# Optimization experiments

Hardware: AMD Instinct MI355X
Metric: run time of the kernel (lower is better)

## Reference

```python
import jax, jax.numpy as jnp
import numpy as np

N = 20000      # nodes
E = 320000     # edges (avg degree 16)
F_IN = 256     # input feature dim
HID = 128      # hidden_channels
H1 = 4         # heads layer 1
ED = 26        # edge feature dim
OUT = 128      # out_channels


def _layernorm(x, g, b, eps=1e-5):
    mu = jnp.mean(x, axis=-1, keepdims=True)
    var = jnp.var(x, axis=-1, keepdims=True)
    return (x - mu) * jax.lax.rsqrt(var + eps) * g + b


def _gatv2(x, src, dst, ea, Wl, bl, Wr, br, We, att, bias, n, heads, c, concat):
    # PyG GATv2Conv: lin_l on source nodes, lin_r on target nodes, lin_edge (no bias)
    xl = (x @ Wl + bl).reshape(n, heads, c)          # [N,H,C] source transform
    xr = (x @ Wr + br).reshape(n, heads, c)          # [N,H,C] target transform
    m = xl[src] + xr[dst] + (ea @ We).reshape(-1, heads, c)  # [E,H,C]
    m = jax.nn.leaky_relu(m, 0.2)
    alpha = jnp.einsum('ehc,hc->eh', m, att)          # [E,H]
    amax = jax.ops.segment_max(alpha, dst, num_segments=n)
    ex = jnp.exp(alpha - amax[dst])
    den = jax.ops.segment_sum(ex, dst, num_segments=n)[dst] + 1e-16
    a = ex / den                                      # scatter-softmax over in-edges
    out = jax.ops.segment_sum(xl[src] * a[:, :, None], dst, num_segments=n)  # [N,H,C]
    out = out.reshape(n, heads * c) if concat else out.mean(axis=1)
    return out + bias


def setup_inputs() -> dict:
    key = jax.random.key(0)
    ks = jax.random.split(key, 30)
    r = lambda k, s, sc=0.05: jax.random.normal(k, s, jnp.float32) * sc
    D1 = HID * H1  # 512
    return {
        'x': r(ks[0], (N, F_IN), 1.0),
        'edge_index': jax.random.randint(ks[1], (2, E), 0, N),
        'edge_attr': r(ks[2], (E, ED), 1.0),
        # conv1 (heads=4, concat)
        'W1l': r(ks[3], (F_IN, D1)), 'b1l': jnp.zeros((D1,), jnp.float32),
        'W1r': r(ks[4], (F_IN, D1)), 'b1r': jnp.zeros((D1,), jnp.float32),
        'We1': r(ks[5], (ED, D1)),
        'att1': r(ks[6], (H1, HID)),
        'bias1': jnp.zeros((D1,), jnp.float32),
        'Wskip1': r(ks[7], (F_IN, D1)), 'bskip1': jnp.zeros((D1,), jnp.float32),
        'g1': jnp.ones((D1,), jnp.float32), 'be1': jnp.zeros((D1,), jnp.float32),
        # conv2 (heads=1, mean)
        'W2l': r(ks[8], (D1, OUT)), 'b2l': jnp.zeros((OUT,), jnp.float32),
        'W2r': r(ks[9], (D1, OUT)), 'b2r': jnp.zeros((OUT,), jnp.float32),
        'We2': r(ks[10], (ED, OUT)),
        'att2': r(ks[11], (1, OUT)),
        'bias2': jnp.zeros((OUT,), jnp.float32),
        'Wskip2': r(ks[12], (D1, OUT)), 'bskip2': jnp.zeros((OUT,), jnp.float32),
        'g2': jnp.ones((OUT,), jnp.float32), 'be2': jnp.zeros((OUT,), jnp.float32),
    }


def reference(x, edge_index, edge_attr, W1l, b1l, W1r, b1r, We1, att1, bias1,
              Wskip1, bskip1, g1, be1, W2l, b2l, W2r, b2r, We2, att2, bias2,
              Wskip2, bskip2, g2, be2):
    src, dst = edge_index[0], edge_index[1]
    h = _gatv2(x, src, dst, edge_attr, W1l, b1l, W1r, b1r, We1, att1, bias1,
               N, H1, HID, True)
    h = h + (x @ Wskip1 + bskip1)
    h = jax.nn.elu(_layernorm(h, g1, be1))  # dropout is identity in eval
    h2 = _gatv2(h, src, dst, edge_attr, W2l, b2l, W2r, b2r, We2, att2, bias2,
                N, 1, OUT, False)
    h2 = h2 + (h @ Wskip2 + bskip2)
    return _layernorm(h2, g2, be2)
```

## Files before the change

kernel.cpp:

```cpp
#include <hip/hip_runtime.h>
#include <hip/hip_bf16.h>

typedef __bf16 bf16;
typedef __bf16 v8bf __attribute__((ext_vector_type(8)));
typedef float f32x4 __attribute__((ext_vector_type(4)));
typedef float f32x2 __attribute__((ext_vector_type(2)));

#define NN 20000
#define EE 320000
#define FIN 256
#define D1 512
#define DOUT 128
#define ED 26

__device__ __forceinline__ float b2f(bf16 x) { return (float)x; }

__device__ __forceinline__ f32x2 ldbf2v(const bf16* p) {
  unsigned int u;
  __builtin_memcpy(&u, p, 4);
  union { unsigned int i; float f; } lo, hi;
  lo.i = (u & 0xffffu) << 16;
  hi.i = u & 0xffff0000u;
  return (f32x2){lo.f, hi.f};
}

__device__ __forceinline__ f32x2 ldf2v(const float* p) {
  f32x2 t;
  __builtin_memcpy(&t, p, 8);
  return t;
}

__device__ __forceinline__ f32x4 ldf4v(const float* p) {
  f32x4 t;
  __builtin_memcpy(&t, p, 16);
  return t;
}

__global__ void zero_k(int* __restrict__ p, int n) {
  int i = blockIdx.x * 256 + threadIdx.x;
  if (i < n) p[i] = 0;
}

__global__ void detflag_k(const int* __restrict__ ei32, int* __restrict__ flag) {
  int i = blockIdx.x * 256 + threadIdx.x;
  int v = (i < EE) ? ei32[2 * i + 1] : 0;
  unsigned long long b = __ballot(v != 0);
  if ((threadIdx.x & 63) == 0 && b) atomicOr(flag, 1);
}

__global__ void conv_k(const void* __restrict__ ei, const int* __restrict__ flag,
                       int* __restrict__ src, int* __restrict__ dst) {
  int i = blockIdx.x * 256 + threadIdx.x;
  if (i >= EE) return;
  int s, d;
  if (*flag == 0) {
    const long long* p = (const long long*)ei;
    s = (int)p[i];
    d = (int)p[EE + i];
  } else {
    const int* p = (const int*)ei;
    s = p[i];
    d = p[EE + i];
  }
  src[i] = min(max(s, 0), NN - 1);
  dst[i] = min(max(d, 0), NN - 1);
}

__global__ void hist_k(const int* __restrict__ dst, int* __restrict__ deg, int n) {
  int e = blockIdx.x * 256 + threadIdx.x;
  if (e < n) atomicAdd(&deg[dst[e]], 1);
}

__global__ __launch_bounds__(1024) void scan_k(const int* __restrict__ deg,
                                               int* __restrict__ offs,
                                               int* __restrict__ cursor, int n) {
  __shared__ int lsum[1024];
  int t = threadIdx.x;
  const int CH = (n + 1023) / 1024;
  int base = t * CH;
  int s = 0;
  for (int i = 0; i < CH; i++) {
    int idx = base + i;
    if (idx < n) s += deg[idx];
  }
  lsum[t] = s;
  __syncthreads();
  for (int o = 1; o < 1024; o <<= 1) {
    int v = (t >= o) ? lsum[t - o] : 0;
    __syncthreads();
    lsum[t] += v;
    __syncthreads();
  }
  int ex = (t == 0) ? 0 : lsum[t - 1];
  for (int i = 0; i < CH; i++) {
    int idx = base + i;
    if (idx < n) {
      offs[idx] = ex;
      cursor[idx] = ex;
      ex += deg[idx];
    }
  }
  if (t == 1023) offs[n] = lsum[1023];
}

__global__ void scatter_k(const int* __restrict__ dst, int* __restrict__ cursor,
                          int* __restrict__ elist, int n) {
  int e = blockIdx.x * 256 + threadIdx.x;
  if (e < n) {
    int p = atomicAdd(&cursor[dst[e]], 1);
    if ((unsigned)p < (unsigned)EE) elist[p] = e;
  }
}

__global__ __launch_bounds__(256) void egather_k(
    const float* __restrict__ eatt, const int* __restrict__ elist,
    const int* __restrict__ srcs, const int* __restrict__ dsts,
    bf16* __restrict__ ea_csr, int* __restrict__ s_csr,
    int* __restrict__ d_csr) {
  __shared__ int e_s[128];
  int tid = threadIdx.x;
  int base = blockIdx.x * 128;
  if (tid < 128) {
    int e = elist[base + tid];
    e = min(max(e, 0), EE - 1);
    e_s[tid] = e;
    s_csr[base + tid] = srcs[e];
    d_csr[base + tid] = dsts[e];
  }
  __syncthreads();
  for (int idx = tid; idx < 128 * 32; idx += 256) {
    int i = idx >> 5, k = idx & 31;
    float v = (k < 26) ? eatt[(size_t)e_s[i] * ED + k] : 0.f;
    ea_csr[(size_t)(base + i) * 32 + k] = (bf16)v;
  }
}

__global__ __launch_bounds__(256) void xpack_k(const float* __restrict__ x,
                                               bf16* __restrict__ xbf,
                                               long long n8) {
  long long i = (long long)blockIdx.x * 256 + threadIdx.x;
  if (i >= n8) return;
  const float* ap = x + i * 8;
  f32x4 u, v;
  __builtin_memcpy(&u, ap, 16);
  __builtin_memcpy(&v, ap + 4, 16);
  v8bf o;
#pragma unroll
  for (int j = 0; j < 4; j++) {
    o[j] = (bf16)u[j];
    o[4 + j] = (bf16)v[j];
  }
  __builtin_memcpy(xbf + i * 8, &o, 16);
}

__global__ __launch_bounds__(256) void packT_k(const float* __restrict__ W,
                                               bf16* __restrict__ Bp,
                                               int Nc, int K) {
  __shared__ float t[32][33];
  int c0 = blockIdx.x * 32, k0 = blockIdx.y * 32;
  int tr = threadIdx.x >> 5, tc = threadIdx.x & 31;
#pragma unroll
  for (int i = 0; i < 32; i += 8)
    t[tr + i][tc] = W[(size_t)(k0 + tr + i) * Nc + c0 + tc];
  __syncthreads();
#pragma unroll
  for (int i = 0; i < 32; i += 8)
    Bp[(size_t)(c0 + tr + i) * K + k0 + tc] = (bf16)t[tc][tr + i];
}

__global__ __launch_bounds__(256) void packWe_k(const float* __restrict__ We,
                                                bf16* __restrict__ Wp, int Nc) {
  int o = blockIdx.x * 256 + threadIdx.x;
  int j = o & 7;
  int lc = (o >> 3) & 15;
  int quad = (o >> 7) & 3;
  int ng = o >> 9;
  int k = quad * 8 + j;
  int col = ng * 16 + lc;
  float v = (k < 26) ? We[(size_t)k * Nc + col] : 0.f;
  Wp[o] = (bf16)v;
}

template <typename TA, typename TO, bool ADD>
__global__ __launch_bounds__(256) void gemm_t(const TA* __restrict__ A,
                                              const float* __restrict__ B,
                                              const float* __restrict__ bias,
                                              TO* out, int Nc, int K) {
  int w = threadIdx.x >> 6;
  int l = threadIdx.x & 63;
  int quad = l >> 4;
  int mrow = blockIdx.y * 16 + (l & 15);
  int col = blockIdx.x * 64 + w * 16 + (l & 15);
  f32x4 acc = {0.f, 0.f, 0.f, 0.f};
  for (int k0 = 0; k0 < K; k0 += 32) {
    int ka = k0 + quad * 8;
    v8bf a, b;
    if constexpr (sizeof(TA) == 4) {
      const float* ap = (const float*)A + (size_t)mrow * K + ka;
#pragma unroll
      for (int j = 0; j < 8; j++) a[j] = (bf16)ap[j];
    } else {
      __builtin_memcpy(&a, (const bf16*)A + (size_t)mrow * K + ka, 16);
    }
#pragma unroll
    for (int j = 0; j < 8; j++) b[j] = (bf16)B[(size_t)(ka + j) * Nc + col];
    acc = __builtin_amdgcn_mfma_f32_16x16x32_bf16(a, b, acc, 0, 0, 0);
  }
  float bb = bias[col];
  int obase = blockIdx.y * 16 + quad * 4;
#pragma unroll
  for (int r = 0; r < 4; r++) {
    size_t idx = (size_t)(obase + r) * Nc + col;
    float v = acc[r] + bb;
    if (ADD) v += (float)out[idx];
    out[idx] = (TO)v;
  }
}

template <typename TA, typename TO>
__global__ __launch_bounds__(256) void gemm2_t(const TA* __restrict__ A,
                                               const float* __restrict__ B0,
                                               const float* __restrict__ B1,
                                               const float* __restrict__ bias0,
                                               const float* __restrict__ bias1,
                                               TO* __restrict__ out0,
                                               TO* __restrict__ out1,
                                               int Nc, int K) {
  int w = threadIdx.x >> 6;
  int l = threadIdx.x & 63;
  int quad = l >> 4;
  int mrow = blockIdx.y * 16 + (l & 15);
  int col = blockIdx.x * 64 + w * 16 + (l & 15);
  f32x4 acc0 = {0.f, 0.f, 0.f, 0.f};
  f32x4 acc1 = {0.f, 0.f, 0.f, 0.f};
  for (int k0 = 0; k0 < K; k0 += 32) {
    int ka = k0 + quad * 8;
    v8bf a, b0, b1;
    if constexpr (sizeof(TA) == 4) {
      const float* ap = (const float*)A + (size_t)mrow * K + ka;
#pragma unroll
      for (int j = 0; j < 8; j++) a[j] = (bf16)ap[j];
    } else {
      __builtin_memcpy(&a, (const bf16*)A + (size_t)mrow * K + ka, 16);
    }
#pragma unroll
    for (int j = 0; j < 8; j++) {
      size_t bi = (size_t)(ka + j) * Nc + col;
      b0[j] = (bf16)B0[bi];
      b1[j] = (bf16)B1[bi];
    }
    acc0 = __builtin_amdgcn_mfma_f32_16x16x32_bf16(a, b0, acc0, 0, 0, 0);
    acc1 = __builtin_amdgcn_mfma_f32_16x16x32_bf16(a, b1, acc1, 0, 0, 0);
  }
  float bb0 = bias0[col], bb1 = bias1[col];
  int obase = blockIdx.y * 16 + quad * 4;
#pragma unroll
  for (int r = 0; r < 4; r++) {
    size_t idx = (size_t)(obase + r) * Nc + col;
    out0[idx] = (TO)(acc0[r] + bb0);
    out1[idx] = (TO)(acc1[r] + bb1);
  }
}

template <typename TA, typename TO>
__global__ __launch_bounds__(256) void gemm3p_t(
    const TA* __restrict__ A, const bf16* __restrict__ Bp,
    const float* __restrict__ bias0, const float* __restrict__ bias1,
    const float* __restrict__ bias2, TO* __restrict__ out0,
    TO* __restrict__ out1, TO* __restrict__ out2, int Nc, int K, int M) {
  int w = threadIdx.x >> 6;
  int l = threadIdx.x & 63;
  int quad = l >> 4, lc = l & 15;
  int col = blockIdx.x * 64 + w * 16 + lc;
  int mbase = blockIdx.y * 64;
  const bf16* b0p = Bp + (size_t)col * K;
  const bf16* b1p = Bp + ((size_t)Nc + col) * K;
  const bf16* b2p = Bp + ((size_t)2 * Nc + col) * K;
  f32x4 acc[4][3];
#pragma unroll
  for (int i = 0; i < 4; i++)
#pragma unroll
    for (int j = 0; j < 3; j++) acc[i][j] = (f32x4){0.f, 0.f, 0.f, 0.f};
  for (int k0 = 0; k0 < K; k0 += 32) {
    int ka = k0 + quad * 8;
    v8bf b0, b1, b2;
    __builtin_memcpy(&b0, b0p + ka, 16);
    __builtin_memcpy(&b1, b1p + ka, 16);
    __builtin_memcpy(&b2, b2p + ka, 16);
#pragma unroll
    for (int ms = 0; ms < 4; ms++) {
      int row = min(mbase + ms * 16 + lc, M - 1);
      v8bf a;
      if constexpr (sizeof(TA) == 4) {
        const float* ap = (const float*)A + (size_t)row * K + ka;
        f32x4 u, v;
        __builtin_memcpy(&u, ap, 16);
        __builtin_memcpy(&v, ap + 4, 16);
#pragma unroll
        for (int j = 0; j < 4; j++) {
          a[j] = (bf16)u[j];
          a[4 + j] = (bf16)v[j];
        }
      } else {
        __builtin_memcpy(&a, (const bf16*)A + (size_t)row * K + ka, 16);
      }
      acc[ms][0] = __builtin_amdgcn_mfma_f32_16x16x32_bf16(a, b0, acc[ms][0], 0, 0, 0);
      acc[ms][1] = __builtin_amdgcn_mfma_f32_16x16x32_bf16(a, b1, acc[ms][1], 0, 0, 0);
      acc[ms][2] = __builtin_amdgcn_mfma_f32_16x16x32_bf16(a, b2, acc[ms][2], 0, 0, 0);
    }
  }
  float bb0 = bias0[col], bb1 = bias1[col], bb2 = bias2[col];
#pragma unroll
  for (int ms = 0; ms < 4; ms++) {
    int ob = mbase + ms * 16 + quad * 4;
#pragma unroll
    for (int r = 0; r < 4; r++) {
      int orow = ob + r;
      if (orow < M) {
        size_t idx = (size_t)orow * Nc + col;
        out0[idx] = (TO)(acc[ms][0][r] + bb0);
        out1[idx] = (TO)(acc[ms][1][r] + bb1);
        out2[idx] = (TO)(acc[ms][2][r] + bb2);
      }
    }
  }
}

__global__ __launch_bounds__(256) void alpha1c_k(
    const bf16* __restrict__ xl, const bf16* __restrict__ xr,
    const bf16* __restrict__ ea_csr, const bf16* __restrict__ Wp,
    const float* __restrict__ att, const int* __restrict__ s_csr,
    const int* __restrict__ d_csr, float* __restrict__ alphap) {
  __shared__ bf16 ea_s[128 * 40];
  int tid = threadIdx.x;
  int w = __builtin_amdgcn_readfirstlane(tid >> 6);
  int l = tid & 63;
  int quad = l >> 4, lc = l & 15;
  int base = blockIdx.x * 128;
  for (int idx = tid; idx < 1024; idx += 256) {
    int i = idx >> 3, k4 = (idx & 7) * 4;
    unsigned long long v;
    __builtin_memcpy(&v, ea_csr + (size_t)(base + i) * 32 + k4, 8);
    __builtin_memcpy(&ea_s[i * 40 + k4], &v, 8);
  }
  int c0 = w * 128;
  v8bf bfrag[8];
  float av[8];
#pragma unroll
  for (int n = 0; n < 8; n++) {
    int col = c0 + n * 16 + lc;
    av[n] = att[col];
    __builtin_memcpy(&bfrag[n],
                     Wp + ((size_t)((w * 8 + n) * 4 + quad) * 16 + lc) * 8, 16);
  }
  __syncthreads();
#pragma unroll 1
  for (int m = 0; m < 8; m++) {
    v8bf afrag;
    __builtin_memcpy(&afrag, &ea_s[(m * 16 + lc) * 40 + quad * 8], 16);
    f32x4 z = {0.f, 0.f, 0.f, 0.f};
    f32x4 acc[8];
#pragma unroll
    for (int n = 0; n < 8; n++)
      acc[n] = __builtin_amdgcn_mfma_f32_16x16x32_bf16(afrag, bfrag[n], z, 0, 0, 0);
    int e0 = base + m * 16 + quad * 4;
    int sA[4], dA[4];
#pragma unroll
    for (int r = 0; r < 4; r++) {
      sA[r] = s_csr[e0 + r];
      dA[r] = d_csr[e0 + r];
    }
    f32x4 pal = {0.f, 0.f, 0.f, 0.f};
#pragma unroll
    for (int n = 0; n < 8; n++) {
      int col = c0 + n * 16 + lc;
#pragma unroll
      for (int r = 0; r < 4; r++) {
        float mm = (float)xl[(size_t)sA[r] * D1 + col] +
                   (float)xr[(size_t)dA[r] * D1 + col] + acc[n][r];
        mm = fmaxf(mm, 0.f) + 0.2f * fminf(mm, 0.f);
        pal[r] += mm * av[n];
      }
    }
#pragma unroll
    for (int o = 1; o < 16; o <<= 1) {
      pal[0] += __shfl_xor(pal[0], o, 64);
      pal[1] += __shfl_xor(pal[1], o, 64);
      pal[2] += __shfl_xor(pal[2], o, 64);
      pal[3] += __shfl_xor(pal[3], o, 64);
    }
    if (lc == 0) {
#pragma unroll
      for (int r = 0; r < 4; r++) alphap[(size_t)(e0 + r) * 4 + w] = pal[r];
    }
  }
}

__global__ __launch_bounds__(256) void alpha2c_k(
    const float* __restrict__ xl, const float* __restrict__ xr,
    const bf16* __restrict__ ea_csr, const bf16* __restrict__ Wp,
    const float* __restrict__ att, const int* __restrict__ s_csr,
    const int* __restrict__ d_csr, float* __restrict__ alphap) {
  __shared__ bf16 ea_s[128 * 40];
  __shared__ float pal_s[4 * 128];
  int tid = threadIdx.x;
  int w = __builtin_amdgcn_readfirstlane(tid >> 6);
  int l = tid & 63;
  int quad = l >> 4, lc = l & 15;
  int base = blockIdx.x * 128;
  for (int idx = tid; idx < 1024; idx += 256) {
    int i = idx >> 3, k4 = (idx & 7) * 4;
    unsigned long long v;
    __builtin_memcpy(&v, ea_csr + (size_t)(base + i) * 32 + k4, 8);
    __builtin_memcpy(&ea_s[i * 40 + k4], &v, 8);
  }
  int c0 = w * 32;
  v8bf bfrag[2];
  float av[2];
#pragma unroll
  for (int n = 0; n < 2; n++) {
    int col = c0 + n * 16 + lc;
    av[n] = att[col];
    __builtin_memcpy(&bfrag[n],
                     Wp + ((size_t)((w * 2 + n) * 4 + quad) * 16 + lc) * 8, 16);
  }
  __syncthreads();
#pragma unroll 1
  for (int m = 0; m < 8; m++) {
    v8bf afrag;
    __builtin_memcpy(&afrag, &ea_s[(m * 16 + lc) * 40 + quad * 8], 16);
    f32x4 z = {0.f, 0.f, 0.f, 0.f};
    f32x4 acc[2];
#pragma unroll
    for (int n = 0; n < 2; n++)
      acc[n] = __builtin_amdgcn_mfma_f32_16x16x32_bf16(afrag, bfrag[n], z, 0, 0, 0);
    int e0 = base + m * 16 + quad * 4;
    int sA[4], dA[4];
#pragma unroll
    for (int r = 0; r < 4; r++) {
      sA[r] = s_csr[e0 + r];
      dA[r] = d_csr[e0 + r];
    }
    f32x4 pal = {0.f, 0.f, 0.f, 0.f};
#pragma unroll
    for (int n = 0; n < 2; n++) {
      int col = c0 + n * 16 + lc;
#pragma unroll
      for (int r = 0; r < 4; r++) {
        float mm = xl[(size_t)sA[r] * DOUT + col] +
                   xr[(size_t)dA[r] * DOUT + col] + acc[n][r];
        mm = fmaxf(mm, 0.f) + 0.2f * fminf(mm, 0.f);
        pal[r] += mm * av[n];
      }
    }
#pragma unroll
    for (int o = 1; o < 16; o <<= 1) {
      pal[0] += __shfl_xor(pal[0], o, 64);
      pal[1] += __shfl_xor(pal[1], o, 64);
      pal[2] += __shfl_xor(pal[2], o, 64);
      pal[3] += __shfl_xor(pal[3], o, 64);
    }
    if (lc == 0) {
      int eb = m * 16 + quad * 4;
#pragma unroll
      for (int r = 0; r < 4; r++) pal_s[w * 128 + eb + r] = pal[r];
    }
  }
  __syncthreads();
  if (tid < 128) {
    float a = pal_s[tid] + pal_s[128 + tid] + pal_s[256 + tid] + pal_s[384 + tid];
    alphap[base + tid] = a;
  }
}

__global__ __launch_bounds__(256) void agg1c_k(
    const bf16* __restrict__ xl, const bf16* __restrict__ skip,
    const float* __restrict__ alphap, const float* __restrict__ bias,
    const float* __restrict__ g, const float* __restrict__ be,
    const int* __restrict__ s_csr, const int* __restrict__ offs,
    bf16* __restrict__ hout) {
  int tid = threadIdx.x;
  int w = tid >> 6, l = tid & 63;
  int node = blockIdx.x * 4 + w;
  if (node >= NN) return;
  int c = l * 8;
  int head = l >> 4;
  int i0 = offs[node], i1 = offs[node + 1];
  i0 = max(0, min(i0, EE));
  i1 = max(i0, min(i1, EE));
  float m = -3.0e38f;
  for (int i = i0 + (l & 15); i < i1; i += 16)
    m = fmaxf(m, alphap[(size_t)i * 4 + head]);
#pragma unroll
  for (int o = 1; o < 16; o <<= 1) m = fmaxf(m, __shfl_xor(m, o, 64));
  float den = 0.f;
  f32x4 a0 = {0.f, 0.f, 0.f, 0.f}, a1 = {0.f, 0.f, 0.f, 0.f};
  int s = 0;
  float al = 0.f;
  if (i0 < i1) {
    s = __builtin_amdgcn_readfirstlane(s_csr[i0]);
    al = alphap[(size_t)i0 * 4 + head];
  }
  for (int i = i0; i < i1; i++) {
    int s_n = s;
    float al_n = al;
    if (i + 1 < i1) {
      s_n = __builtin_amdgcn_readfirstlane(s_csr[i + 1]);
      al_n = alphap[(size_t)(i + 1) * 4 + head];
    }
    float pr = __expf(al - m);
    den += pr;
    v8bf xv;
    __builtin_memcpy(&xv, xl + (size_t)s * D1 + c, 16);
#pragma unroll
    for (int j = 0; j < 4; j++) {
      a0[j] += pr * (float)xv[j];
      a1[j] += pr * (float)xv[4 + j];
    }
    s = s_n;
    al = al_n;
  }
  float inv = 1.f / (den + 1e-16f);
  v8bf skv;
  __builtin_memcpy(&skv, skip + (size_t)node * D1 + c, 16);
  f32x4 bv0 = ldf4v(bias + c), bv1 = ldf4v(bias + c + 4);
  float o[8];
#pragma unroll
  for (int j = 0; j < 4; j++) {
    o[j] = a0[j] * inv + bv0[j] + (float)skv[j];
    o[4 + j] = a1[j] * inv + bv1[j] + (float)skv[4 + j];
  }
  float s1 = 0.f, s2 = 0.f;
#pragma unroll
  for (int j = 0; j < 8; j++) {
    s1 += o[j];
    s2 += o[j] * o[j];
  }
#pragma unroll
  for (int of = 32; of; of >>= 1) {
    s1 += __shfl_xor(s1, of, 64);
    s2 += __shfl_xor(s2, of, 64);
  }
  float mu = s1 * (1.f / 512.f);
  float var = fmaxf(s2 * (1.f / 512.f) - mu * mu, 0.f);
  float rs = rsqrtf(var + 1e-5f);
  f32x4 gv0 = ldf4v(g + c), gv1 = ldf4v(g + c + 4);
  f32x4 ev0 = ldf4v(be + c), ev1 = ldf4v(be + c + 4);
  v8bf hv;
#pragma unroll
  for (int j = 0; j < 4; j++) {
    float y0 = (o[j] - mu) * rs * gv0[j] + ev0[j];
    float y1 = (o[4 + j] - mu) * rs * gv1[j] + ev1[j];
    y0 = y0 > 0.f ? y0 : __expf(fminf(y0, 0.f)) - 1.f;
    y1 = y1 > 0.f ? y1 : __expf(fminf(y1, 0.f)) - 1.f;
    hv[j] = (bf16)y0;
    hv[4 + j] = (bf16)y1;
  }
  __builtin_memcpy(hout + (size_t)node * D1 + c, &hv, 16);
}

__global__ __launch_bounds__(256) void agg2c_k(
    const float* __restrict__ xl, const float* __restrict__ skip,
    const float* __restrict__ alphap, const float* __restrict__ bias,
    const float* __restrict__ g, const float* __restrict__ be,
    const int* __restrict__ s_csr, const int* __restrict__ offs,
    float* __restrict__ outp) {
  int tid = threadIdx.x;
  int w = tid >> 6, l = tid & 63;
  int node = blockIdx.x * 4 + w;
  if (node >= NN) return;
  int c = 2 * l;
  int i0 = offs[node], i1 = offs[node + 1];
  i0 = max(0, min(i0, EE));
  i1 = max(i0, min(i1, EE));
  float m = -3.0e38f;
  for (int i = i0 + l; i < i1; i += 64) m = fmaxf(m, alphap[i]);
#pragma unroll
  for (int o = 32; o; o >>= 1) m = fmaxf(m, __shfl_xor(m, o, 64));
  float den = 0.f;
  f32x2 acc = {0.f, 0.f};
  int s = 0;
  float al = 0.f;
  if (i0 < i1) {
    s = __builtin_amdgcn_readfirstlane(s_csr[i0]);
    al = alphap[i0];
  }
  for (int i = i0; i < i1; i++) {
    int s_n = s;
    float al_n = al;
    if (i + 1 < i1) {
      s_n = __builtin_amdgcn_readfirstlane(s_csr[i + 1]);
      al_n = alphap[i + 1];
    }
    float pr = __expf(al - m);
    den += pr;
    f32x2 xv = ldf2v(xl + (size_t)s * DOUT + c);
    acc += (f32x2){pr, pr} * xv;
    s = s_n;
    al = al_n;
  }
  float inv = 1.f / (den + 1e-16f);
  f32x2 sk = ldf2v(skip + (size_t)node * DOUT + c);
  float o0 = acc.x * inv + bias[c] + sk.x;
  float o1 = acc.y * inv + bias[c + 1] + sk.y;
  float s1 = o0 + o1, s2 = o0 * o0 + o1 * o1;
#pragma unroll
  for (int of = 32; of; of >>= 1) {
    s1 += __shfl_xor(s1, of, 64);
    s2 += __shfl_xor(s2, of, 64);
  }
  float mu = s1 * (1.f / 128.f);
  float var = fmaxf(s2 * (1.f / 128.f) - mu * mu, 0.f);
  float rs = rsqrtf(var + 1e-5f);
  outp[(size_t)node * DOUT + c] = (o0 - mu) * rs * g[c] + be[c];
  outp[(size_t)node * DOUT + c + 1] = (o1 - mu) * rs * g[c + 1] + be[c + 1];
}

__global__ __launch_bounds__(256) void alpha1_k(
    const bf16* __restrict__ xl, const bf16* __restrict__ xr,
    const float* __restrict__ eatt, const float* __restrict__ We,
    const float* __restrict__ att, const int* __restrict__ srcs,
    const int* __restrict__ dsts, float* __restrict__ alpha) {
  __shared__ bf16 ea_s[128 * 40];
  int tid = threadIdx.x;
  int w = __builtin_amdgcn_readfirstlane(tid >> 6);
  int l = tid & 63;
  int quad = l >> 4, lc = l & 15;
  int base = blockIdx.x * 128;
  for (int i = tid; i < 128 * 32; i += 256) {
    int e = i >> 5, k = i & 31;
    float v = (k < 26) ? eatt[(size_t)(base + e) * ED + k] : 0.f;
    ea_s[e * 40 + k] = (bf16)v;
  }
  int c0 = w * 128;
  v8bf bfrag[8];
  float av[8];
#pragma unroll
  for (int n = 0; n < 8; n++) {
    int col = c0 + n * 16 + lc;
    av[n] = att[col];
#pragma unroll
    for (int j = 0; j < 8; j++) {
      int k = quad * 8 + j;
      bfrag[n][j] = (k < 26) ? (bf16)We[(size_t)k * D1 + col] : (bf16)0.f;
    }
  }
  __syncthreads();
#pragma unroll 1
  for (int m = 0; m < 8; m++) {
    v8bf afrag;
    __builtin_memcpy(&afrag, &ea_s[(m * 16 + lc) * 40 + quad * 8], 16);
    f32x4 z = {0.f, 0.f, 0.f, 0.f};
    f32x4 acc[8];
#pragma unroll
    for (int n = 0; n < 8; n++)
      acc[n] = __builtin_amdgcn_mfma_f32_16x16x32_bf16(afrag, bfrag[n], z, 0, 0, 0);
    int e0 = base + m * 16 + quad * 4;
    int sA[4], dA[4];
#pragma unroll
    for (int r = 0; r < 4; r++) {
      sA[r] = srcs[e0 + r];
      dA[r] = dsts[e0 + r];
    }
    f32x4 pal = {0.f, 0.f, 0.f, 0.f};
#pragma unroll
    for (int n = 0; n < 8; n++) {
      int col = c0 + n * 16 + lc;
#pragma unroll
      for (int r = 0; r < 4; r++) {
        float mm = (float)xl[(size_t)sA[r] * D1 + col] +
                   (float)xr[(size_t)dA[r] * D1 + col] + acc[n][r];
        mm = fmaxf(mm, 0.f) + 0.2f * fminf(mm, 0.f);
        pal[r] += mm * av[n];
      }
    }
#pragma unroll
    for (int o = 1; o < 16; o <<= 1) {
      pal[0] += __shfl_xor(pal[0], o, 64);
      pal[1] += __shfl_xor(pal[1], o, 64);
      pal[2] += __shfl_xor(pal[2], o, 64);
      pal[3] += __shfl_xor(pal[3], o, 64);
    }
    if (lc == 0) {
#pragma unroll
      for (int r = 0; r < 4; r++) alpha[(size_t)(e0 + r) * 4 + w] = pal[r];
    }
  }
}

__global__ __launch_bounds__(256) void alpha2_k(
    const float* __restrict__ xl, const float* __restrict__ xr,
    const float* __restrict__ eatt, const float* __restrict__ We,
    const float* __restrict__ att, const int* __restrict__ srcs,
    const int* __restrict__ dsts, float* __restrict__ alpha) {
  __shared__ bf16 ea_s[128 * 40];
  __shared__ float pal_s[4 * 128];
  int tid = threadIdx.x;
  int w = __builtin_amdgcn_readfirstlane(tid >> 6);
  int l = tid & 63;
  int quad = l >> 4, lc = l & 15;
  int base = blockIdx.x * 128;
  for (int i = tid; i < 128 * 32; i += 256) {
    int e = i >> 5, k = i & 31;
    float v = (k < 26) ? eatt[(size_t)(base + e) * ED + k] : 0.f;
    ea_s[e * 40 + k] = (bf16)v;
  }
  int c0 = w * 32;
  v8bf bfrag[2];
  float av[2];
#pragma unroll
  for (int n = 0; n < 2; n++) {
    int col = c0 + n * 16 + lc;
    av[n] = att[col];
#pragma unroll
    for (int j = 0; j < 8; j++) {
      int k = quad * 8 + j;
      bfrag[n][j] = (k < 26) ? (bf16)We[(size_t)k * DOUT + col] : (bf16)0.f;
    }
  }
  __syncthreads();
#pragma unroll 1
  for (int m = 0; m < 8; m++) {
    v8bf afrag;
    __builtin_memcpy(&afrag, &ea_s[(m * 16 + lc) * 40 + quad * 8], 16);
    f32x4 z = {0.f, 0.f, 0.f, 0.f};
    f32x4 acc[2];
#pragma unroll
    for (int n = 0; n < 2; n++)
      acc[n] = __builtin_amdgcn_mfma_f32_16x16x32_bf16(afrag, bfrag[n], z, 0, 0, 0);
    int e0 = base + m * 16 + quad * 4;
    int sA[4], dA[4];
#pragma unroll
    for (int r = 0; r < 4; r++) {
      sA[r] = srcs[e0 + r];
      dA[r] = dsts[e0 + r];
    }
    f32x4 pal = {0.f, 0.f, 0.f, 0.f};
#pragma unroll
    for (int n = 0; n < 2; n++) {
      int col = c0 + n * 16 + lc;
#pragma unroll
      for (int r = 0; r < 4; r++) {
        float mm = xl[(size_t)sA[r] * DOUT + col] +
                   xr[(size_t)dA[r] * DOUT + col] + acc[n][r];
        mm = fmaxf(mm, 0.f) + 0.2f * fminf(mm, 0.f);
        pal[r] += mm * av[n];
      }
    }
#pragma unroll
    for (int o = 1; o < 16; o <<= 1) {
      pal[0] += __shfl_xor(pal[0], o, 64);
      pal[1] += __shfl_xor(pal[1], o, 64);
      pal[2] += __shfl_xor(pal[2], o, 64);
      pal[3] += __shfl_xor(pal[3], o, 64);
    }
    if (lc == 0) {
      int eb = m * 16 + quad * 4;
#pragma unroll
      for (int r = 0; r < 4; r++) pal_s[w * 128 + eb + r] = pal[r];
    }
  }
  __syncthreads();
  if (tid < 128) {
    float a = pal_s[tid] + pal_s[128 + tid] + pal_s[256 + tid] + pal_s[384 + tid];
    alpha[base + tid] = a;
  }
}

__global__ __launch_bounds__(256) void agg1_k(
    const bf16* __restrict__ xl, const bf16* __restrict__ skip,
    const float* __restrict__ alpha, const float* __restrict__ bias,
    const float* __restrict__ g, const float* __restrict__ be,
    const int* __restrict__ srcs, const int* __restrict__ offs,
    const int* __restrict__ elist, bf16* __restrict__ hout) {
  int tid = threadIdx.x;
  int w = tid >> 6, l = tid & 63;
  int node = blockIdx.x * 4 + w;
  if (node >= NN) return;
  int c = l * 8;
  int head = l >> 4;
  int i0 = offs[node], i1 = offs[node + 1];
  i0 = max(0, min(i0, EE));
  i1 = max(i0, min(i1, EE));
  float m = -3.0e38f;
  for (int i = i0; i < i1; i++) {
    int e = __builtin_amdgcn_readfirstlane(elist[i]);
    m = fmaxf(m, alpha[(size_t)e * 4 + head]);
  }
  float den = 0.f;
  f32x4 a0 = {0.f, 0.f, 0.f, 0.f}, a1 = {0.f, 0.f, 0.f, 0.f};
  int s = 0;
  float al = 0.f;
  if (i0 < i1) {
    int e = __builtin_amdgcn_readfirstlane(elist[i0]);
    s = __builtin_amdgcn_readfirstlane(srcs[e]);
    al = alpha[(size_t)e * 4 + head];
  }
  for (int i = i0; i < i1; i++) {
    int s_n = s;
    float al_n = al;
    if (i + 1 < i1) {
      int e = __builtin_amdgcn_readfirstlane(elist[i + 1]);
      s_n = __builtin_amdgcn_readfirstlane(srcs[e]);
      al_n = alpha[(size_t)e * 4 + head];
    }
    float pr = __expf(al - m);
    den += pr;
    v8bf xv;
    __builtin_memcpy(&xv, xl + (size_t)s * D1 + c, 16);
#pragma unroll
    for (int j = 0; j < 4; j++) {
      a0[j] += pr * (float)xv[j];
      a1[j] += pr * (float)xv[4 + j];
    }
    s = s_n;
    al = al_n;
  }
  float inv = 1.f / (den + 1e-16f);
  v8bf skv;
  __builtin_memcpy(&skv, skip + (size_t)node * D1 + c, 16);
  f32x4 bv0 = ldf4v(bias + c), bv1 = ldf4v(bias + c + 4);
  float o[8];
#pragma unroll
  for (int j = 0; j < 4; j++) {
    o[j] = a0[j] * inv + bv0[j] + (float)skv[j];
    o[4 + j] = a1[j] * inv + bv1[j] + (float)skv[4 + j];
  }
  float s1 = 0.f, s2 = 0.f;
#pragma unroll
  for (int j = 0; j < 8; j++) {
    s1 += o[j];
    s2 += o[j] * o[j];
  }
#pragma unroll
  for (int of = 32; of; of >>= 1) {
    s1 += __shfl_xor(s1, of, 64);
    s2 += __shfl_xor(s2, of, 64);
  }
  float mu = s1 * (1.f / 512.f);
  float var = fmaxf(s2 * (1.f / 512.f) - mu * mu, 0.f);
  float rs = rsqrtf(var + 1e-5f);
  f32x4 gv0 = ldf4v(g + c), gv1 = ldf4v(g + c + 4);
  f32x4 ev0 = ldf4v(be + c), ev1 = ldf4v(be + c + 4);
  v8bf hv;
#pragma unroll
  for (int j = 0; j < 4; j++) {
    float y0 = (o[j] - mu) * rs * gv0[j] + ev0[j];
    float y1 = (o[4 + j] - mu) * rs * gv1[j] + ev1[j];
    y0 = y0 > 0.f ? y0 : __expf(fminf(y0, 0.f)) - 1.f;
    y1 = y1 > 0.f ? y1 : __expf(fminf(y1, 0.f)) - 1.f;
    hv[j] = (bf16)y0;
    hv[4 + j] = (bf16)y1;
  }
  __builtin_memcpy(hout + (size_t)node * D1 + c, &hv, 16);
}

__global__ __launch_bounds__(256) void agg2_k(
    const float* __restrict__ xl, const float* __restrict__ skip,
    const float* __restrict__ alpha, const float* __restrict__ bias,
    const float* __restrict__ g, const float* __restrict__ be,
    const int* __restrict__ srcs, const int* __restrict__ offs,
    const int* __restrict__ elist, float* __restrict__ outp) {
  int tid = threadIdx.x;
  int w = tid >> 6, l = tid & 63;
  int node = blockIdx.x * 4 + w;
  if (node >= NN) return;
  int c = 2 * l;
  int i0 = offs[node], i1 = offs[node + 1];
  i0 = max(0, min(i0, EE));
  i1 = max(i0, min(i1, EE));
  float m = -3.0e38f;
  for (int i = i0; i < i1; i++) {
    int e = __builtin_amdgcn_readfirstlane(elist[i]);
    m = fmaxf(m, alpha[e]);
  }
  float den = 0.f;
  f32x2 acc = {0.f, 0.f};
  int s = 0;
  float al = 0.f;
  if (i0 < i1) {
    int e = __builtin_amdgcn_readfirstlane(elist[i0]);
    s = __builtin_amdgcn_readfirstlane(srcs[e]);
    al = alpha[e];
  }
  for (int i = i0; i < i1; i++) {
    int s_n = s;
    float al_n = al;
    if (i + 1 < i1) {
      int e = __builtin_amdgcn_readfirstlane(elist[i + 1]);
      s_n = __builtin_amdgcn_readfirstlane(srcs[e]);
      al_n = alpha[e];
    }
    float pr = __expf(al - m);
    den += pr;
    f32x2 xv = ldf2v(xl + (size_t)s * DOUT + c);
    acc += (f32x2){pr, pr} * xv;
    s = s_n;
    al = al_n;
  }
  float inv = 1.f / (den + 1e-16f);
  f32x2 sk = ldf2v(skip + (size_t)node * DOUT + c);
  float o0 = acc.x * inv + bias[c] + sk.x;
  float o1 = acc.y * inv + bias[c + 1] + sk.y;
  float s1 = o0 + o1, s2 = o0 * o0 + o1 * o1;
#pragma unroll
  for (int of = 32; of; of >>= 1) {
    s1 += __shfl_xor(s1, of, 64);
    s2 += __shfl_xor(s2, of, 64);
  }
  float mu = s1 * (1.f / 128.f);
  float var = fmaxf(s2 * (1.f / 128.f) - mu * mu, 0.f);
  float rs = rsqrtf(var + 1e-5f);
  outp[(size_t)node * DOUT + c] = (o0 - mu) * rs * g[c] + be[c];
  outp[(size_t)node * DOUT + c + 1] = (o1 - mu) * rs * g[c + 1] + be[c + 1];
}

__global__ __launch_bounds__(256) void l1_agg(
    const bf16* __restrict__ xl, const bf16* xr,
    const float* __restrict__ eatt, const float* __restrict__ We,
    const float* __restrict__ att, const float* __restrict__ bias,
    const int* __restrict__ srcs, const int* __restrict__ offs,
    const int* __restrict__ elist, bf16* hout) {
  int node = blockIdx.x;
  int tid = threadIdx.x;
  int w = tid >> 6, l = tid & 63;
  int c = w * 128 + 2 * l;
  f32x2 we[ED];
#pragma unroll
  for (int j = 0; j < ED; j++) {
    we[j] = (f32x2){We[(size_t)j * D1 + c], We[(size_t)j * D1 + c + 1]};
  }
  f32x2 av = ldf2v(att + c);
  f32x2 rv = ldbf2v(xr + (size_t)node * D1 + c);
  float m = -3.0e38f, den = 0.f;
  f32x2 acc = {0.f, 0.f};
  int i0 = offs[node], i1 = offs[node + 1];
  i0 = max(0, min(i0, EE));
  i1 = max(i0, min(i1, EE));
  int e = 0, s = 0;
  if (i0 < i1) {
    e = __builtin_amdgcn_readfirstlane(elist[i0]);
    s = __builtin_amdgcn_readfirstlane(srcs[e]);
  }
  for (int i = i0; i < i1; i++) {
    int e_n = e, s_n = s;
    if (i + 1 < i1) {
      e_n = __builtin_amdgcn_readfirstlane(elist[i + 1]);
      s_n = __builtin_amdgcn_readfirstlane(srcs[e_n]);
    }
    f32x2 xv = ldbf2v(xl + (size_t)s * D1 + c);
    const float* ear = eatt + (size_t)e * ED;
    f32x2 et = {0.f, 0.f};
#pragma unroll
    for (int j = 0; j < ED; j += 2) {
      f32x2 t = ldf2v(ear + j);
      et += (f32x2){t.x, t.x} * we[j];
      et += (f32x2){t.y, t.y} * we[j + 1];
    }
    f32x2 mm = xv + rv + et;
    f32x2 pos = {fmaxf(mm.x, 0.f), fmaxf(mm.y, 0.f)};
    f32x2 neg = {fminf(mm.x, 0.f), fminf(mm.y, 0.f)};
    mm = pos + 0.2f * neg;
    float al = mm.x * av.x + mm.y * av.y;
#pragma unroll
    for (int o = 32; o; o >>= 1) al += __shfl_xor(al, o, 64);
    float nm = fmaxf(m, al);
    float sc = __expf(m - nm);
    float pr = __expf(al - nm);
    den = den * sc + pr;
    acc = acc * sc + (f32x2){pr, pr} * xv;
    m = nm;
    e = e_n;
    s = s_n;
  }
  float inv = 1.f / (den + 1e-16f);
  hout[(size_t)node * D1 + c] = (bf16)(acc.x * inv + bias[c]);
  hout[(size_t)node * D1 + c + 1] = (bf16)(acc.y * inv + bias[c + 1]);
}

__global__ __launch_bounds__(256) void l2_agg(
    const float* __restrict__ xl, const float* xr,
    const float* __restrict__ eatt, const float* __restrict__ We,
    const float* __restrict__ att, const float* __restrict__ bias,
    const int* __restrict__ srcs, const int* __restrict__ offs,
    const int* __restrict__ elist, float* hout) {
  int tid = threadIdx.x;
  int w = tid >> 6, l = tid & 63;
  int node = blockIdx.x * 4 + w;
  if (node >= NN) return;
  int c = 2 * l;
  f32x2 we[ED];
#pragma unroll
  for (int j = 0; j < ED; j++) {
    we[j] = (f32x2){We[(size_t)j * DOUT + c], We[(size_t)j * DOUT + c + 1]};
  }
  f32x2 av = ldf2v(att + c);
  f32x2 rv = ldf2v(xr + (size_t)node * DOUT + c);
  float m = -3.0e38f, den = 0.f;
  f32x2 acc = {0.f, 0.f};
  int i0 = offs[node], i1 = offs[node + 1];
  i0 = max(0, min(i0, EE));
  i1 = max(i0, min(i1, EE));
  int e = 0, s = 0;
  if (i0 < i1) {
    e = __builtin_amdgcn_readfirstlane(elist[i0]);
    s = __builtin_amdgcn_readfirstlane(srcs[e]);
  }
  for (int i = i0; i < i1; i++) {
    int e_n = e, s_n = s;
    if (i + 1 < i1) {
      e_n = __builtin_amdgcn_readfirstlane(elist[i + 1]);
      s_n = __builtin_amdgcn_readfirstlane(srcs[e_n]);
    }
    f32x2 xv = ldf2v(xl + (size_t)s * DOUT + c);
    const float* ear = eatt + (size_t)e * ED;
    f32x2 et = {0.f, 0.f};
#pragma unroll
    for (int j = 0; j < ED; j += 2) {
      f32x2 t = ldf2v(ear + j);
      et += (f32x2){t.x, t.x} * we[j];
      et += (f32x2){t.y, t.y} * we[j + 1];
    }
    f32x2 mm = xv + rv + et;
    f32x2 pos = {fmaxf(mm.x, 0.f), fmaxf(mm.y, 0.f)};
    f32x2 neg = {fminf(mm.x, 0.f), fminf(mm.y, 0.f)};
    mm = pos + 0.2f * neg;
    float al = mm.x * av.x + mm.y * av.y;
#pragma unroll
    for (int o = 32; o; o >>= 1) al += __shfl_xor(al, o, 64);
    float nm = fmaxf(m, al);
    float sc = __expf(m - nm);
    float pr = __expf(al - nm);
    den = den * sc + pr;
    acc = acc * sc + (f32x2){pr, pr} * xv;
    m = nm;
    e = e_n;
    s = s_n;
  }
  float inv = 1.f / (den + 1e-16f);
  hout[(size_t)node * DOUT + c] = acc.x * inv + bias[c];
  hout[(size_t)node * DOUT + c + 1] = acc.y * inv + bias[c + 1];
}

__global__ __launch_bounds__(256) void lnelu_k(bf16* buf,
                                               const float* __restrict__ g,
                                               const float* __restrict__ be) {
  int node = blockIdx.x, tid = threadIdx.x;
  int w = tid >> 6, l = tid & 63;
  int c = tid * 2;
  f32x2 o = ldbf2v(buf + (size_t)node * D1 + c);
  float s1 = o.x + o.y, s2 = o.x * o.x + o.y * o.y;
#pragma unroll
  for (int of = 32; of; of >>= 1) {
    s1 += __shfl_xor(s1, of, 64);
    s2 += __shfl_xor(s2, of, 64);
  }
  __shared__ float r1[4], r2[4];
  if (l == 0) { r1[w] = s1; r2[w] = s2; }
  __syncthreads();
  float S1 = r1[0] + r1[1] + r1[2] + r1[3];
  float S2 = r2[0] + r2[1] + r2[2] + r2[3];
  float mu = S1 * (1.f / 512.f);
  float var = fmaxf(S2 * (1.f / 512.f) - mu * mu, 0.f);
  float rs = rsqrtf(var + 1e-5f);
  float y0 = (o.x - mu) * rs * g[c] + be[c];
  float y1 = (o.y - mu) * rs * g[c + 1] + be[c + 1];
  y0 = y0 > 0.f ? y0 : __expf(fminf(y0, 0.f)) - 1.f;
  y1 = y1 > 0.f ? y1 : __expf(fminf(y1, 0.f)) - 1.f;
  buf[(size_t)node * D1 + c] = (bf16)y0;
  buf[(size_t)node * D1 + c + 1] = (bf16)y1;
}

__global__ __launch_bounds__(256) void ln128_k(const float* __restrict__ buf,
                                               const float* __restrict__ g,
                                               const float* __restrict__ be,
                                               float* __restrict__ outp) {
  int tid = threadIdx.x;
  int w = tid >> 6, l = tid & 63;
  int node = blockIdx.x * 4 + w;
  if (node >= NN) return;
  int c = 2 * l;
  f32x2 o = ldf2v(buf + (size_t)node * DOUT + c);
  float s1 = o.x + o.y, s2 = o.x * o.x + o.y * o.y;
#pragma unroll
  for (int of = 32; of; of >>= 1) {
    s1 += __shfl_xor(s1, of, 64);
    s2 += __shfl_xor(s2, of, 64);
  }
  float mu = s1 * (1.f / 128.f);
  float var = fmaxf(s2 * (1.f / 128.f) - mu * mu, 0.f);
  float rs = rsqrtf(var + 1e-5f);
  outp[(size_t)node * DOUT + c] = (o.x - mu) * rs * g[c] + be[c];
  outp[(size_t)node * DOUT + c + 1] = (o.y - mu) * rs * g[c + 1] + be[c + 1];
}

extern "C" void kernel_launch(void* const* d_in, const int* in_sizes, int n_in,
                              void* d_out, int out_size, void* d_ws, size_t ws_size,
                              hipStream_t stream) {
  const float* x = (const float*)d_in[0];
  const void* ei = d_in[1];
  const float* eattr = (const float*)d_in[2];
  const float* W1l = (const float*)d_in[3];
  const float* b1l = (const float*)d_in[4];
  const float* W1r = (const float*)d_in[5];
  const float* b1r = (const float*)d_in[6];
  const float* We1 = (const float*)d_in[7];
  const float* att1 = (const float*)d_in[8];
  const float* bias1 = (const float*)d_in[9];
  const float* Wsk1 = (const float*)d_in[10];
  const float* bsk1 = (const float*)d_in[11];
  const float* g1 = (const float*)d_in[12];
  const float* be1 = (const float*)d_in[13];
  const float* W2l = (const float*)d_in[14];
  const float* b2l = (const float*)d_in[15];
  const float* W2r = (const float*)d_in[16];
  const float* b2r = (const float*)d_in[17];
  const float* We2 = (const float*)d_in[18];
  const float* att2 = (const float*)d_in[19];
  const float* bias2 = (const float*)d_in[20];
  const float* Wsk2 = (const float*)d_in[21];
  const float* bsk2 = (const float*)d_in[22];
  const float* g2 = (const float*)d_in[23];
  const float* be2 = (const float*)d_in[24];

  char* p = (char*)d_ws;
  size_t off = 0;
  auto carve = [&](size_t bytes) {
    void* r = p + off;
    off = (off + bytes + 255) & ~(size_t)255;
    return r;
  };
  int* flag = (int*)carve(sizeof(int));
  int* srcD = (int*)carve(EE * sizeof(int));
  int* dstD = (int*)carve(EE * sizeof(int));
  int* deg = (int*)carve(NN * sizeof(int));
  int* offs = (int*)carve((NN + 1) * sizeof(int));
  int* cursor = (int*)carve(NN * sizeof(int));
  int* elist = (int*)carve(EE * sizeof(int));
  bf16* bufA = (bf16*)carve((size_t)NN * D1 * 2);
  bf16* bufB = (bf16*)carve((size_t)NN * D1 * 2);
  size_t base_need = off;
  bf16* bufC = (bf16*)carve((size_t)NN * D1 * 2);
  bool fused = (off <= ws_size);
  bf16* eacsr = (bf16*)carve((size_t)EE * 32 * 2);
  int* s_csr = (int*)carve(EE * sizeof(int));
  int* d_csr = (int*)carve(EE * sizeof(int));
  bool fused2 = (off <= ws_size);
  bf16* xbf = (bf16*)carve((size_t)NN * FIN * 2);
  bool fused3 = (off <= ws_size);

  float* q0 = (float*)bufA;
  float* q1 = q0 + (size_t)NN * DOUT;
  float* sk2 = (float*)bufC;
  float* alph1 = (float*)d_out;
  float* alph2 = (float*)bufB;
  bf16* W1p = (bf16*)((char*)d_out + 5120000);
  bf16* W2p = W1p + (size_t)3 * D1 * FIN;
  bf16* Wep1 = W2p + (size_t)3 * DOUT * D1;
  bf16* Wep2 = Wep1 + 16384;

  zero_k<<<1, 256, 0, stream>>>(flag, 1);
  detflag_k<<<(EE + 255) / 256, 256, 0, stream>>>((const int*)ei, flag);
  conv_k<<<(EE + 255) / 256, 256, 0, stream>>>(ei, flag, srcD, dstD);

  zero_k<<<(NN + 255) / 256, 256, 0, stream>>>(deg, NN);
  hist_k<<<(EE + 255) / 256, 256, 0, stream>>>(dstD, deg, EE);
  scan_k<<<1, 1024, 0, stream>>>(deg, offs, cursor, NN);
  scatter_k<<<(EE + 255) / 256, 256, 0, stream>>>(dstD, cursor, elist, EE);

  if (fused) {
    packT_k<<<dim3(D1 / 32, FIN / 32), 256, 0, stream>>>(W1l, W1p, D1, FIN);
    packT_k<<<dim3(D1 / 32, FIN / 32), 256, 0, stream>>>(
        W1r, W1p + (size_t)D1 * FIN, D1, FIN);
    packT_k<<<dim3(D1 / 32, FIN / 32), 256, 0, stream>>>(
        Wsk1, W1p + (size_t)2 * D1 * FIN, D1, FIN);
    packT_k<<<dim3(DOUT / 32, D1 / 32), 256, 0, stream>>>(W2l, W2p, DOUT, D1);
    packT_k<<<dim3(DOUT / 32, D1 / 32), 256, 0, stream>>>(
        W2r, W2p + (size_t)DOUT * D1, DOUT, D1);
    packT_k<<<dim3(DOUT / 32, D1 / 32), 256, 0, stream>>>(
        Wsk2, W2p + (size_t)2 * DOUT * D1, DOUT, D1);
    packWe_k<<<64, 256, 0, stream>>>(We1, Wep1, D1);
    packWe_k<<<16, 256, 0, stream>>>(We2, Wep2, DOUT);
    if (fused3) {
      const long long n8 = (long long)NN * FIN / 8;
      xpack_k<<<(unsigned)((n8 + 255) / 256), 256, 0, stream>>>(x, xbf, n8);
      gemm3p_t<bf16, bf16><<<dim3(D1 / 64, (NN + 63) / 64), 256, 0, stream>>>(
          xbf, W1p, b1l, b1r, bsk1, bufA, bufB, bufC, D1, FIN, NN);
    } else {
      gemm3p_t<float, bf16><<<dim3(D1 / 64, (NN + 63) / 64), 256, 0, stream>>>(
          x, W1p, b1l, b1r, bsk1, bufA, bufB, bufC, D1, FIN, NN);
    }
    if (fused2) {
      egather_k<<<EE / 128, 256, 0, stream>>>(eattr, elist, srcD, dstD,
                                              eacsr, s_csr, d_csr);
      alpha1c_k<<<EE / 128, 256, 0, stream>>>(bufA, bufB, eacsr, Wep1, att1,
                                              s_csr, d_csr, alph1);
      agg1c_k<<<(NN + 3) / 4, 256, 0, stream>>>(bufA, bufC, alph1, bias1, g1,
                                                be1, s_csr, offs, bufB);
      gemm3p_t<bf16, float><<<dim3(DOUT / 64, (NN + 63) / 64), 256, 0, stream>>>(
          bufB, W2p, b2l, b2r, bsk2, q0, q1, sk2, DOUT, D1, NN);
      alpha2c_k<<<EE / 128, 256, 0, stream>>>(q0, q1, eacsr, Wep2, att2,
                                              s_csr, d_csr, alph2);
      agg2c_k<<<(NN + 3) / 4, 256, 0, stream>>>(q0, sk2, alph2, bias2, g2, be2,
                                                s_csr, offs, (float*)d_out);
    } else {
      alpha1_k<<<EE / 128, 256, 0, stream>>>(bufA, bufB, eattr, We1, att1,
                                             srcD, dstD, alph1);
      agg1_k<<<(NN + 3) / 4, 256, 0, stream>>>(bufA, bufC, alph1, bias1, g1,
                                               be1, srcD, offs, elist, bufB);
      gemm3p_t<bf16, float><<<dim3(DOUT / 64, (NN + 63) / 64), 256, 0, stream>>>(
          bufB, W2p, b2l, b2r, bsk2, q0, q1, sk2, DOUT, D1, NN);
      alpha2_k<<<EE / 128, 256, 0, stream>>>(q0, q1, eattr, We2, att2,
                                             srcD, dstD, alph2);
      agg2_k<<<(NN + 3) / 4, 256, 0, stream>>>(q0, sk2, alph2, bias2, g2, be2,
                                               srcD, offs, elist, (float*)d_out);
    }
  } else {
    (void)base_need;
    gemm2_t<float, bf16><<<dim3(D1 / 64, NN / 16), 256, 0, stream>>>(
        x, W1l, W1r, b1l, b1r, bufA, bufB, D1, FIN);
    l1_agg<<<NN, 256, 0, stream>>>(bufA, bufB, eattr, We1, att1, bias1,
                                   srcD, offs, elist, bufB);
    gemm_t<float, bf16, true><<<dim3(D1 / 64, NN / 16), 256, 0, stream>>>(
        x, Wsk1, bsk1, bufB, D1, FIN);
    lnelu_k<<<NN, 256, 0, stream>>>(bufB, g1, be1);
    gemm2_t<bf16, float><<<dim3(DOUT / 64, NN / 16), 256, 0, stream>>>(
        bufB, W2l, W2r, b2l, b2r, q0, q1, DOUT, D1);
    l2_agg<<<(NN + 3) / 4, 256, 0, stream>>>(q0, q1, eattr, We2, att2, bias2,
                                             srcD, offs, elist, q1);
    gemm_t<bf16, float, true><<<dim3(DOUT / 64, NN / 16), 256, 0, stream>>>(
        bufB, Wsk2, bsk2, q1, DOUT, D1);
    ln128_k<<<(NN + 3) / 4, 256, 0, stream>>>(q1, g2, be2, (float*)d_out);
  }

  (void)in_sizes; (void)n_in; (void)out_size;
}
```

Before: 625.6 us.

## Merge preprocessing kernels: fuse conv+histogram, scatter+edge gather, and all weight packing

Cuts the number of small preprocessing launches. Edge-index conversion now also builds the degree histogram, and the CSR scatter writes edge attributes and src/dst in the same pass. All weight transposes, We packing and x conversion run in one multi-role kernel. This removes launch overhead and a second pass over the edge list. In exchange, the edge-attribute gather is now done per thread with scattered 64-byte writes and uncoalesced 104-byte row reads.

After: 596.3 us, median of 2. 4.7% less time.

```diff
diff --git a/kernel.cpp b/kernel.cpp
--- a/kernel.cpp
+++ b/kernel.cpp
@@ -39,6 +39,12 @@
 __global__ void zero_k(int* __restrict__ p, int n) {
   int i = blockIdx.x * 256 + threadIdx.x;
   if (i < n) p[i] = 0;
+}
+
+__global__ void zero2_k(int* __restrict__ deg, int* __restrict__ flag) {
+  int i = blockIdx.x * 256 + threadIdx.x;
+  if (i < NN) deg[i] = 0;
+  if (i == 0) *flag = 0;
 }
 
 __global__ void detflag_k(const int* __restrict__ ei32, int* __restrict__ flag) {
@@ -66,6 +72,28 @@
   dst[i] = min(max(d, 0), NN - 1);
 }
 
+__global__ void conv_hist_k(const void* __restrict__ ei,
+                            const int* __restrict__ flag, int* __restrict__ src,
+                            int* __restrict__ dst, int* __restrict__ deg) {
+  int i = blockIdx.x * 256 + threadIdx.x;
+  if (i >= EE) return;
+  int s, d;
+  if (*flag == 0) {
+    const long long* p = (const long long*)ei;
+    s = (int)p[i];
+    d = (int)p[EE + i];
+  } else {
+    const int* p = (const int*)ei;
+    s = p[i];
+    d = p[EE + i];
+  }
+  s = min(max(s, 0), NN - 1);
+  d = min(max(d, 0), NN - 1);
+  src[i] = s;
+  dst[i] = d;
+  atomicAdd(&deg[d], 1);
+}
+
 __global__ void hist_k(const int* __restrict__ dst, int* __restrict__ deg, int n) {
   int e = blockIdx.x * 256 + threadIdx.x;
   if (e < n) atomicAdd(&deg[dst[e]], 1);
@@ -112,73 +140,97 @@
   }
 }
 
-__global__ __launch_bounds__(256) void egather_k(
-    const float* __restrict__ eatt, const int* __restrict__ elist,
-    const int* __restrict__ srcs, const int* __restrict__ dsts,
-    bf16* __restrict__ ea_csr, int* __restrict__ s_csr,
-    int* __restrict__ d_csr) {
-  __shared__ int e_s[128];
+__global__ __launch_bounds__(256) void scatter_eg_k(
+    const float* __restrict__ eattr, const int* __restrict__ srcs,
+    const int* __restrict__ dsts, int* __restrict__ cursor,
+    int* __restrict__ elist, bf16* __restrict__ ea_csr,
+    int* __restrict__ s_csr, int* __restrict__ d_csr) {
+  int e = blockIdx.x * 256 + threadIdx.x;
+  if (e >= EE) return;
+  int s = srcs[e], d = dsts[e];
+  int p = atomicAdd(&cursor[d], 1);
+  if ((unsigned)p >= (unsigned)EE) return;
+  elist[p] = e;
+  s_csr[p] = s;
+  d_csr[p] = d;
+  const float* er = eattr + (size_t)e * ED;
+  bf16 row[32];
+#pragma unroll
+  for (int k = 0; k < 26; k++) row[k] = (bf16)er[k];
+#pragma unroll
+  for (int k = 26; k < 32; k++) row[k] = (bf16)0.f;
+  __builtin_memcpy(ea_csr + (size_t)p * 32, row, 64);
+}
+
+__global__ __launch_bounds__(256) void packall_k(
+    const float* __restrict__ W1l, const float* __restrict__ W1r,
+    const float* __restrict__ Wsk1, const float* __restrict__ W2l,
+    const float* __restrict__ W2r, const float* __restrict__ Wsk2,
+    const float* __restrict__ We1, const float* __restrict__ We2,
+    const float* __restrict__ x, bf16* __restrict__ W1p,
+    bf16* __restrict__ W2p, bf16* __restrict__ Wep1, bf16* __restrict__ Wep2,
+    bf16* __restrict__ xbf) {
+  __shared__ float t[32][33];
+  int b = blockIdx.x;
   int tid = threadIdx.x;
-  int base = blockIdx.x * 128;
-  if (tid < 128) {
-    int e = elist[base + tid];
-    e = min(max(e, 0), EE - 1);
-    e_s[tid] = e;
-    s_csr[base + tid] = srcs[e];
-    d_csr[base + tid] = dsts[e];
-  }
-  __syncthreads();
-  for (int idx = tid; idx < 128 * 32; idx += 256) {
-    int i = idx >> 5, k = idx & 31;
-    float v = (k < 26) ? eatt[(size_t)e_s[i] * ED + k] : 0.f;
-    ea_csr[(size_t)(base + i) * 32 + k] = (bf16)v;
-  }
-}
-
-__global__ __launch_bounds__(256) void xpack_k(const float* __restrict__ x,
-                                               bf16* __restrict__ xbf,
-                                               long long n8) {
-  long long i = (long long)blockIdx.x * 256 + threadIdx.x;
-  if (i >= n8) return;
-  const float* ap = x + i * 8;
-  f32x4 u, v;
-  __builtin_memcpy(&u, ap, 16);
-  __builtin_memcpy(&v, ap + 4, 16);
-  v8bf o;
-#pragma unroll
-  for (int j = 0; j < 4; j++) {
-    o[j] = (bf16)u[j];
-    o[4 + j] = (bf16)v[j];
-  }
-  __builtin_memcpy(xbf + i * 8, &o, 16);
-}
-
-__global__ __launch_bounds__(256) void packT_k(const float* __restrict__ W,
-                                               bf16* __restrict__ Bp,
-                                               int Nc, int K) {
-  __shared__ float t[32][33];
-  int c0 = blockIdx.x * 32, k0 = blockIdx.y * 32;
-  int tr = threadIdx.x >> 5, tc = threadIdx.x & 31;
-#pragma unroll
-  for (int i = 0; i < 32; i += 8)
-    t[tr + i][tc] = W[(size_t)(k0 + tr + i) * Nc + c0 + tc];
-  __syncthreads();
-#pragma unroll
-  for (int i = 0; i < 32; i += 8)
-    Bp[(size_t)(c0 + tr + i) * K + k0 + tc] = (bf16)t[tc][tr + i];
-}
-
-__global__ __launch_bounds__(256) void packWe_k(const float* __restrict__ We,
-                                                bf16* __restrict__ Wp, int Nc) {
-  int o = blockIdx.x * 256 + threadIdx.x;
-  int j = o & 7;
-  int lc = (o >> 3) & 15;
-  int quad = (o >> 7) & 3;
-  int ng = o >> 9;
-  int k = quad * 8 + j;
-  int col = ng * 16 + lc;
-  float v = (k < 26) ? We[(size_t)k * Nc + col] : 0.f;
-  Wp[o] = (bf16)v;
+  if (b < 576) {
+    const float* W;
+    bf16* Bp;
+    int Nc, K, bx, by;
+    if (b < 384) {
+      int j = b / 128, tt = b % 128;
+      W = j == 0 ? W1l : (j == 1 ? W1r : Wsk1);
+      Bp = W1p + (size_t)j * D1 * FIN;
+      Nc = D1;
+      K = FIN;
+      bx = tt % 16;
+      by = tt / 16;
+    } else {
+      int j = (b - 384) / 64, tt = (b - 384) % 64;
+      W = j == 0 ? W2l : (j == 1 ? W2r : Wsk2);
+      Bp = W2p + (size_t)j * DOUT * D1;
+      Nc = DOUT;
+      K = D1;
+      bx = tt % 4;
+      by = tt / 4;
+    }
+    int c0 = bx * 32, k0 = by * 32;
+    int tr = tid >> 5, tc = tid & 31;
+#pragma unroll
+    for (int i = 0; i < 32; i += 8)
+      t[tr + i][tc] = W[(size_t)(k0 + tr + i) * Nc + c0 + tc];
+    __syncthreads();
+#pragma unroll
+    for (int i = 0; i < 32; i += 8)
+      Bp[(size_t)(c0 + tr + i) * K + k0 + tc] = (bf16)t[tc][tr + i];
+  } else if (b < 656) {
+    const float* We;
+    bf16* Wp;
+    int Nc, blk;
+    if (b < 640) {
+      We = We1; Wp = Wep1; Nc = D1; blk = b - 576;
+    } else {
+      We = We2; Wp = Wep2; Nc = DOUT; blk = b - 640;
+    }
+    int o = blk * 256 + tid;
+    int j = o & 7, lc = (o >> 3) & 15, quad = (o >> 7) & 3, ng = o >> 9;
+    int k = quad * 8 + j, col = ng * 16 + lc;
+    float v = (k < 26) ? We[(size_t)k * Nc + col] : 0.f;
+    Wp[o] = (bf16)v;
+  } else {
+    long long i = (long long)(b - 656) * 256 + tid;
+    const float* ap = x + i * 8;
+    f32x4 u, v;
+    __builtin_memcpy(&u, ap, 16);
+    __builtin_memcpy(&v, ap + 4, 16);
+    v8bf o;
+#pragma unroll
+    for (int j = 0; j < 4; j++) {
+      o[j] = (bf16)u[j];
+      o[4 + j] = (bf16)v[j];
+    }
+    __builtin_memcpy(xbf + i * 8, &o, 16);
+  }
 }
 
 template <typename TA, typename TO, bool ADD>
@@ -1159,31 +1211,27 @@
   bf16* Wep1 = W2p + (size_t)3 * DOUT * D1;
   bf16* Wep2 = Wep1 + 16384;
 
-  zero_k<<<1, 256, 0, stream>>>(flag, 1);
-  detflag_k<<<(EE + 255) / 256, 256, 0, stream>>>((const int*)ei, flag);
-  conv_k<<<(EE + 255) / 256, 256, 0, stream>>>(ei, flag, srcD, dstD);
-
-  zero_k<<<(NN + 255) / 256, 256, 0, stream>>>(deg, NN);
-  hist_k<<<(EE + 255) / 256, 256, 0, stream>>>(dstD, deg, EE);
-  scan_k<<<1, 1024, 0, stream>>>(deg, offs, cursor, NN);
-  scatter_k<<<(EE + 255) / 256, 256, 0, stream>>>(dstD, cursor, elist, EE);
+  if (fused2) {
+    zero2_k<<<(NN + 255) / 256, 256, 0, stream>>>(deg, flag);
+    detflag_k<<<(EE + 255) / 256, 256, 0, stream>>>((const int*)ei, flag);
+    conv_hist_k<<<(EE + 255) / 256, 256, 0, stream>>>(ei, flag, srcD, dstD, deg);
+    scan_k<<<1, 1024, 0, stream>>>(deg, offs, cursor, NN);
+    scatter_eg_k<<<(EE + 255) / 256, 256, 0, stream>>>(
+        eattr, srcD, dstD, cursor, elist, eacsr, s_csr, d_csr);
+  } else {
+    zero_k<<<1, 256, 0, stream>>>(flag, 1);
+    detflag_k<<<(EE + 255) / 256, 256, 0, stream>>>((const int*)ei, flag);
+    conv_k<<<(EE + 255) / 256, 256, 0, stream>>>(ei, flag, srcD, dstD);
+    zero_k<<<(NN + 255) / 256, 256, 0, stream>>>(deg, NN);
+    hist_k<<<(EE + 255) / 256, 256, 0, stream>>>(dstD, deg, EE);
+    scan_k<<<1, 1024, 0, stream>>>(deg, offs, cursor, NN);
+    scatter_k<<<(EE + 255) / 256, 256, 0, stream>>>(dstD, cursor, elist, EE);
+  }
 
   if (fused) {
-    packT_k<<<dim3(D1 / 32, FIN / 32), 256, 0, stream>>>(W1l, W1p, D1, FIN);
-    packT_k<<<dim3(D1 / 32, FIN / 32), 256, 0, stream>>>(
-        W1r, W1p + (size_t)D1 * FIN, D1, FIN);
-    packT_k<<<dim3(D1 / 32, FIN / 32), 256, 0, stream>>>(
-        Wsk1, W1p + (size_t)2 * D1 * FIN, D1, FIN);
-    packT_k<<<dim3(DOUT / 32, D1 / 32), 256, 0, stream>>>(W2l, W2p, DOUT, D1);
-    packT_k<<<dim3(DOUT / 32, D1 / 32), 256, 0, stream>>>(
-        W2r, W2p + (size_t)DOUT * D1, DOUT, D1);
-    packT_k<<<dim3(DOUT / 32, D1 / 32), 256, 0, stream>>>(
-        Wsk2, W2p + (size_t)2 * DOUT * D1, DOUT, D1);
-    packWe_k<<<64, 256, 0, stream>>>(We1, Wep1, D1);
-    packWe_k<<<16, 256, 0, stream>>>(We2, Wep2, DOUT);
+    packall_k<<<fused3 ? 3156 : 656, 256, 0, stream>>>(
+        W1l, W1r, Wsk1, W2l, W2r, Wsk2, We1, We2, x, W1p, W2p, Wep1, Wep2, xbf);
     if (fused3) {
-      const long long n8 = (long long)NN * FIN / 8;
-      xpack_k<<<(unsigned)((n8 + 255) / 256), 256, 0, stream>>>(x, xbf, n8);
       gemm3p_t<bf16, bf16><<<dim3(D1 / 64, (NN + 63) / 64), 256, 0, stream>>>(
           xbf, W1p, b1l, b1r, bsk1, bufA, bufB, bufC, D1, FIN, NN);
     } else {
@@ -1191,8 +1239,6 @@
           x, W1p, b1l, b1r, bsk1, bufA, bufB, bufC, D1, FIN, NN);
     }
     if (fused2) {
-      egather_k<<<EE / 128, 256, 0, stream>>>(eattr, elist, srcD, dstD,
-                                              eacsr, s_csr, d_csr);
       alpha1c_k<<<EE / 128, 256, 0, stream>>>(bufA, bufB, eacsr, Wep1, att1,
                                               s_csr, d_csr, alph1);
       agg1c_k<<<(NN + 3) / 4, 256, 0, stream>>>(bufA, bufC, alph1, bias1, g1,
```
